# Optimization experiments

Hardware: AMD Instinct MI355X
Metric: run time of the kernel (lower is better)

The kernel has to match this reference:

```python
import jax, jax.numpy as jnp
import numpy as np
from jax import lax

V = 500000  # vocab
B = 4096    # batch_num (fixed at init via h0/c0)
E = 64      # embed_size_word
H = 64      # lstm hidden


def setup_inputs() -> dict:
    key = jax.random.key(0)
    ks = iter(jax.random.split(key, 40))
    nrm = lambda *s: 0.1 * jax.random.normal(next(ks), s, dtype=jnp.float32)
    x = jax.random.randint(next(ks), (912, B), 0, V).astype(jnp.float32)
    return dict(
        x=x,
        word_embed=nrm(V, E),
        lstm_Wih=nrm(4, 4 * H, E), lstm_Whh=nrm(4, 4 * H, H),
        lstm_bih=nrm(4, 4 * H), lstm_bhh=nrm(4, 4 * H),
        h0=nrm(4, B, H), c0=nrm(4, B, H),
        w_l=nrm(4, H, H), b_l=jnp.zeros((4, H, 1), jnp.float32),
        conv1_w=nrm(12, 1, 2, E), conv1_b=jnp.zeros((12,), jnp.float32),
        lin1_w=nrm(64, 24), lin1_b=jnp.zeros((64,), jnp.float32),
        conv2_w=nrm(12, 1, 2, E), conv2_b=jnp.zeros((12,), jnp.float32),
        lin2_w=nrm(64, 24), lin2_b=jnp.zeros((64,), jnp.float32),
        wide_w=nrm(64, 81), wide_b=jnp.zeros((64, 1), jnp.float32),
        cq_w=nrm(64, 64 * 7), cq_b=jnp.zeros((64, 1), jnp.float32),
        cqu_w=nrm(64, 128), cqu_b=jnp.zeros((64, 1), jnp.float32),
        dw_w=nrm(1, 64), dw_b=jnp.zeros((1, 1), jnp.float32),
    )


def _masked_mean(terms_f, table):
    # terms_f: [rows, B] float ids. Faithful to torch: L = sum(sign(all terms)),
    # L = L if L > 1 else 1, then mean over first min(L, rows) rows.
    rows = terms_f.shape[0]
    emb = table[terms_f.astype(jnp.int32)]                    # [rows, B, E]
    n = jnp.sum(jnp.sign(terms_f))
    L = jnp.minimum(jnp.where(n > 1, n, 1.0), float(rows))
    mask = (jnp.arange(rows, dtype=jnp.float32) < L)[:, None, None]
    return jnp.sum(emb * mask, axis=0) / L                    # [B, E]


def _lstm_last(x_seq, h0, c0, Wih, Whh, bih, bhh):
    # PyTorch LSTM (i,f,g,o gate order); returns last-step output h_T. x_seq: [T,B,E]
    def step(carry, xt):
        h, c = carry
        g = xt @ Wih.T + h @ Whh.T + bih + bhh                # [B, 4H]
        i, f, gg, o = jnp.split(g, 4, axis=-1)
        c = jax.nn.sigmoid(f) * c + jax.nn.sigmoid(i) * jnp.tanh(gg)
        h = jax.nn.sigmoid(o) * jnp.tanh(c)
        return (h, c), None
    (h, _), _ = lax.scan(step, (h0, c0), x_seq)
    return h                                                  # [B, H]


def reference(x, word_embed, lstm_Wih, lstm_Whh, lstm_bih, lstm_bhh, h0, c0, w_l, b_l,
              conv1_w, conv1_b, lin1_w, lin1_b, conv2_w, conv2_b, lin2_w, lin2_b,
              wide_w, wide_b, cq_w, cq_b, cqu_w, cqu_b, dw_w, dw_b):
    Bn = x.shape[1]
    wide_feat = x[:81]
    user_item_seq = x[81:276]
    query_feat = x[276:292]
    user_query_seq = x[292:462]
    query_item_query = x[462:562]
    user_query_item = x[562:662]
    user_item_query = x[662:812]
    query_user_item = x[812:]

    q_sum = _masked_mean(query_feat[:10], word_embed).T       # [64, B]

    def step_means(seg, chunk, term_rows):
        # split seg into 5 chunks of `chunk` rows, embed first `term_rows` rows per chunk
        chunks = seg.reshape(5, chunk, Bn)[:, :term_rows]     # [5, term_rows, B]
        return jax.vmap(lambda t: _masked_mean(t, word_embed))(chunks)  # [5, B, E]

    def lstm_stream(steps, i):
        h = _lstm_last(steps, h0[i], c0[i], lstm_Wih[i], lstm_Whh[i], lstm_bih[i], lstm_bhh[i])
        return jnp.tanh(w_l[i] @ h.T + b_l[i])                # [64, B]

    s1 = lstm_stream(step_means(user_item_seq[-65:], 13, 10), 0)
    s2 = lstm_stream(step_means(user_item_query[:50], 10, 5), 1)
    s3 = lstm_stream(step_means(user_query_item[-50:], 10, 5), 2)
    s4 = lstm_stream(step_means(user_query_seq[-65:], 13, 10), 3)

    def cnn_stream(steps, cw, cb, lw, lb):
        xi = steps.transpose(1, 0, 2)[:, None]                # [B, 1, 5, E]
        y = lax.conv_general_dilated(xi, cw, (1, 1), 'VALID',
                dimension_numbers=('NCHW', 'OIHW', 'NCHW')) + cb[None, :, None, None]
        y = jax.nn.relu(y)                                    # [B, 12, 4, 1]
        y = lax.reduce_window(y, -jnp.inf, lax.max, (1, 1, 2, 1), (1, 1, 2, 1), 'VALID')
        y = y.transpose(0, 2, 3, 1).reshape(Bn, 24)           # [B, 2*1*12]
        return jax.nn.relu(y @ lw.T + lb).T                   # [64, B]

    c1 = cnn_stream(step_means(query_item_query[-50:], 10, 5), conv1_w, conv1_b, lin1_w, lin1_b)
    c2 = cnn_stream(step_means(query_user_item[-50:], 10, 5), conv2_w, conv2_b, lin2_w, lin2_b)

    wide = jnp.tanh(wide_w @ wide_feat + wide_b)              # [64, B]
    q = jnp.tanh(cq_w @ jnp.concatenate([q_sum, s1, s2, s3, s4, c1, c2], 0) + cq_b)
    qw = jnp.tanh(cqu_w @ jnp.concatenate([q, wide], 0) + cqu_b)
    return dw_w @ qw + dw_b                                   # [1, B] logits
```

## Files before the change

### kernel.cpp

```cpp
#include <hip/hip_runtime.h>
#include <math.h>

#define BN 4096
typedef unsigned short u16;
typedef unsigned int   u32;
typedef short bfx8 __attribute__((ext_vector_type(8)));
typedef float fx4  __attribute__((ext_vector_type(4)));

__device__ const int c_base[31] = {
  276,
  211, 224, 237, 250, 263,
  662, 672, 682, 692, 702,
  612, 622, 632, 642, 652,
  397, 410, 423, 436, 449,
  512, 522, 532, 542, 552,
  862, 872, 882, 892, 902
};
__device__ const int c_rows[31] = {
  10,
  10,10,10,10,10,
  5,5,5,5,5,
  5,5,5,5,5,
  10,10,10,10,10,
  5,5,5,5,5,
  5,5,5,5,5
};

__device__ __forceinline__ u16 f2bf(float f){
  u32 u = __float_as_uint(f);
  return (u16)((u + 0x7FFFu + ((u >> 16) & 1u)) >> 16);
}
__device__ __forceinline__ float bf2f(u16 h){ return __uint_as_float(((u32)h) << 16); }
__device__ __forceinline__ float4 ld4(const float* p){ return *(const float4*)p; }
__device__ __forceinline__ float sigf(float v){ return 1.0f / (1.0f + __expf(-v)); }

extern "C" __global__ __launch_bounds__(256)
void setup_kernel(const float* __restrict__ x, int* __restrict__ cnt,
                  const float* __restrict__ Wih, const float* __restrict__ Whh,
                  const float* __restrict__ wl,  const float* __restrict__ bih,
                  const float* __restrict__ bhh,
                  const float* __restrict__ cqw, const float* __restrict__ cquw,
                  const float* __restrict__ ww,  const float* __restrict__ l1w,
                  const float* __restrict__ l2w,
                  u16* __restrict__ Wcb, u16* __restrict__ wlb,
                  float* __restrict__ bias_sum,
                  float* __restrict__ cqwT, float* __restrict__ cquwT,
                  float* __restrict__ wwT,  float* __restrict__ lwT){
  __shared__ int red[256];
  if (blockIdx.x < 248){
    const int c = blockIdx.x >> 3, part = blockIdx.x & 7;
    const int base = c_base[c], rows = c_rows[c];
    const int n_per = rows * 512;
    const int start = part * n_per;
    int s = 0;
    for (int i = start + threadIdx.x; i < start + n_per; i += 256){
      float v = x[(size_t)(base + (i >> 12)) * BN + (i & 4095)];
      s += (v > 0.f) ? 1 : ((v < 0.f) ? -1 : 0);
    }
    red[threadIdx.x] = s; __syncthreads();
    for (int off = 128; off > 0; off >>= 1){
      if (threadIdx.x < off) red[threadIdx.x] += red[threadIdx.x + off];
      __syncthreads();
    }
    if (threadIdx.x == 0) atomicAdd(&cnt[c], red[0]);
    return;
  }
  int idx = (blockIdx.x - 248) * 256 + threadIdx.x;
  if (idx < 131072){
    int s = idx >> 15, rem = idx & 32767, n = rem >> 7, k = rem & 127;
    float v = (k < 64) ? Wih[s*16384 + n*64 + k] : Whh[s*16384 + n*64 + (k-64)];
    Wcb[idx] = f2bf(v);
  } else if (idx < 147456){
    int j = idx - 131072;
    wlb[j] = f2bf(wl[j]);
  } else if (idx < 148480){
    int j = idx - 147456;
    bias_sum[j] = bih[j] + bhh[j];
  } else if (idx < 177152){
    int j = idx - 148480;
    int k = j >> 6, m = j & 63;
    cqwT[j] = cqw[m*448 + k];
  } else if (idx < 185344){
    int j = idx - 177152;
    int k = j >> 6, m = j & 63;
    cquwT[j] = cquw[m*128 + k];
  } else if (idx < 190528){
    int j = idx - 185344;
    int k = j >> 6, m = j & 63;
    wwT[j] = ww[m*81 + k];
  } else if (idx < 193600){
    int j = idx - 190528;
    int cs = j >= 1536;
    int r = j - (cs ? 1536 : 0);
    int k = r >> 6, m = r & 63;
    lwT[j] = (cs ? l2w : l1w)[m*24 + k];
  }
}

template<int ROWS>
__device__ __forceinline__ void means_body(const float* __restrict__ x,
                                           const float* __restrict__ we,
                                           float L, int base, int b0, int lane,
                                           float* m){
  float a0 = 0.f, a1 = 0.f, a2 = 0.f, a3 = 0.f;
  #pragma unroll
  for (int r = 0; r < ROWS; ++r){
    float4 iv = ld4(x + (size_t)(base + r) * BN + b0);
    float wr = ((float)r < L) ? 1.f : 0.f;
    a0 += wr * we[(size_t)(int)iv.x * 64 + lane];
    a1 += wr * we[(size_t)(int)iv.y * 64 + lane];
    a2 += wr * we[(size_t)(int)iv.z * 64 + lane];
    a3 += wr * we[(size_t)(int)iv.w * 64 + lane];
  }
  m[0] = a0 / L; m[1] = a1 / L; m[2] = a2 / L; m[3] = a3 / L;
}

extern "C" __global__ __launch_bounds__(256)
void means_kernel(const float* __restrict__ x, const float* __restrict__ we,
                  const int* __restrict__ cnt, u16* __restrict__ Mbf){
  const int c = blockIdx.x >> 8, tile = blockIdx.x & 255;
  const int w = threadIdx.x >> 6, lane = threadIdx.x & 63;
  const int b0 = tile * 16 + w * 4;
  const int base = c_base[c], rows = c_rows[c];
  const float L = fminf(fmaxf((float)cnt[c], 1.f), (float)rows);
  float m[4];
  if (rows == 5) means_body<5>(x, we, L, base, b0, lane, m);
  else          means_body<10>(x, we, L, base, b0, lane, m);
  #pragma unroll
  for (int j = 0; j < 4; ++j)
    Mbf[((size_t)c * BN + b0 + j) * 64 + lane] = f2bf(m[j]);
}

extern "C" __global__ __launch_bounds__(256, 1)
void lstm_kernel(const u16* __restrict__ Wcb, const u16* __restrict__ wlb,
                 const float* __restrict__ bias_sum, const u16* __restrict__ Mbf,
                 const float* __restrict__ h0, const float* __restrict__ c0,
                 const float* __restrict__ bl, float* __restrict__ S){
  __shared__ u16 Xh[64][136];

  const int tid = threadIdx.x, w = tid >> 6, lane = tid & 63;
  const int quad = lane >> 4, l0 = lane & 15;
  const int st = blockIdx.x & 3, tile = blockIdx.x >> 2, b0 = tile * 64;
  const int brow = 16 * w + l0;
  const u16* Wc = Wcb + (size_t)st * 32768;

  fx4 bias4[16];
  #pragma unroll
  for (int mt = 0; mt < 16; ++mt)
    bias4[mt] = *(const fx4*)(bias_sum + st*256 + mt*16 + quad*4);

  float cst[4][4];
  #pragma unroll
  for (int dc = 0; dc < 4; ++dc){
    float4 v = ld4(c0 + ((size_t)st*BN + b0 + brow)*64 + dc*16 + quad*4);
    cst[dc][0]=v.x; cst[dc][1]=v.y; cst[dc][2]=v.z; cst[dc][3]=v.w;
  }
  {
    const float* hp = h0 + ((size_t)st*BN + b0 + brow)*64 + quad*16;
    #pragma unroll
    for (int i = 0; i < 4; ++i){
      float4 v = ld4(hp + i*4);
      u32* dst = (u32*)&Xh[brow][64 + quad*16 + i*4];
      dst[0] = (u32)f2bf(v.x) | ((u32)f2bf(v.y) << 16);
      dst[1] = (u32)f2bf(v.z) | ((u32)f2bf(v.w) << 16);
    }
  }

  for (int t = 0; t < 5; ++t){
    {
      const u16* src = Mbf + ((size_t)(1 + st*5 + t)*BN + b0 + brow)*64 + quad*16;
      *(uint4*)&Xh[brow][quad*16]     = *(const uint4*)src;
      *(uint4*)&Xh[brow][quad*16 + 8] = *(const uint4*)(src + 8);
    }
    __syncthreads();

    fx4 acc[16];
    #pragma unroll
    for (int mt = 0; mt < 16; ++mt) acc[mt] = bias4[mt];
    #pragma unroll
    for (int kc = 0; kc < 4; ++kc){
      bfx8 bfr = *(const bfx8*)&Xh[brow][kc*32 + quad*8];
      #pragma unroll
      for (int mt = 0; mt < 16; ++mt){
        bfx8 afr = *(const bfx8*)(Wc + (size_t)(mt*16 + l0)*128 + kc*32 + quad*8);
        acc[mt] = __builtin_amdgcn_mfma_f32_16x16x32_bf16(afr, bfr, acc[mt], 0, 0, 0);
      }
    }
    #pragma unroll
    for (int dc = 0; dc < 4; ++dc){
      u16 hv[4];
      #pragma unroll
      for (int r = 0; r < 4; ++r){
        float ig = sigf(acc[dc][r]);
        float fg = sigf(acc[4 + dc][r]);
        float gg = tanhf(acc[8 + dc][r]);
        float og = sigf(acc[12 + dc][r]);
        float cc = fg * cst[dc][r] + ig * gg;
        cst[dc][r] = cc;
        hv[r] = f2bf(og * tanhf(cc));
      }
      u32* dst = (u32*)&Xh[brow][64 + dc*16 + quad*4];
      dst[0] = (u32)hv[0] | ((u32)hv[1] << 16);
      dst[1] = (u32)hv[2] | ((u32)hv[3] << 16);
    }
    __syncthreads();
  }

  fx4 acc2[4];
  #pragma unroll
  for (int mt = 0; mt < 4; ++mt){ acc2[mt].x=0.f; acc2[mt].y=0.f; acc2[mt].z=0.f; acc2[mt].w=0.f; }
  #pragma unroll
  for (int kc = 0; kc < 2; ++kc){
    bfx8 bfr = *(const bfx8*)&Xh[brow][64 + kc*32 + quad*8];
    #pragma unroll
    for (int mt = 0; mt < 4; ++mt){
      bfx8 afr = *(const bfx8*)(wlb + (size_t)st*4096 + (size_t)(mt*16 + l0)*64 + kc*32 + quad*8);
      acc2[mt] = __builtin_amdgcn_mfma_f32_16x16x32_bf16(afr, bfr, acc2[mt], 0, 0, 0);
    }
  }
  #pragma unroll
  for (int mt = 0; mt < 4; ++mt){
    fx4 blv = *(const fx4*)(bl + st*64 + mt*16 + quad*4);
    fx4 o;
    o.x = tanhf(acc2[mt].x + blv.x);
    o.y = tanhf(acc2[mt].y + blv.y);
    o.z = tanhf(acc2[mt].z + blv.z);
    o.w = tanhf(acc2[mt].w + blv.w);
    *(fx4*)(S + ((size_t)st*BN + b0 + brow)*64 + mt*16 + quad*4) = o;
  }
}

extern "C" __global__ __launch_bounds__(256)
void final_kernel(
    const float* __restrict__ x,   const u16* __restrict__ Mbf,
    const float* __restrict__ S,
    const float* __restrict__ c1w, const float* __restrict__ c1b,
    const float* __restrict__ c2w, const float* __restrict__ c2b,
    const float* __restrict__ l1b, const float* __restrict__ l2b,
    const float* __restrict__ wwT, const float* __restrict__ wb,
    const float* __restrict__ cqwT,const float* __restrict__ cqb,
    const float* __restrict__ cquwT,const float* __restrict__ cqub,
    const float* __restrict__ lwT, const float* __restrict__ dww,
    const float* __restrict__ dwb, float* __restrict__ out)
{
  __shared__ float cb[448][9];
  __shared__ float qwin[128][9];
  __shared__ float sm[5][64][9];
  __shared__ float co[48][9];
  __shared__ float cwS[12][130];
  __shared__ float red[32][8];

  const int tid = threadIdx.x;
  const int b   = tid & 7;
  const int mg  = tid >> 3;
  const int b0  = blockIdx.x * 8;

  {
    const int e = tid & 63, rr = tid >> 6;
    #pragma unroll
    for (int i = 0; i < 2; ++i){
      const int bb = rr*2 + i;
      cb[e][bb] = bf2f(Mbf[(size_t)(b0 + bb)*64 + e]);
      #pragma unroll
      for (int s = 0; s < 4; ++s)
        cb[64 + s*64 + e][bb] = S[((size_t)s*BN + b0 + bb)*64 + e];
    }
  }

  {
    float a0 = wb[mg*2], a1 = wb[mg*2+1];
    #pragma unroll 4
    for (int k = 0; k < 81; ++k){
      float xv = x[(size_t)k*BN + b0 + b];
      float2 wv = *(const float2*)(wwT + k*64 + mg*2);
      a0 += wv.x * xv; a1 += wv.y * xv;
    }
    qwin[64 + mg*2][b]     = tanhf(a0);
    qwin[64 + mg*2 + 1][b] = tanhf(a1);
  }

  for (int cs = 0; cs < 2; ++cs){
    const float* cw    = cs ? c2w : c1w;
    const float* cbias = cs ? c2b : c1b;
    const float* lb    = cs ? l2b : l1b;

    __syncthreads();
    {
      const int e = tid & 63, rr = tid >> 6;
      #pragma unroll
      for (int t = 0; t < 5; ++t)
        #pragma unroll
        for (int i = 0; i < 2; ++i){
          const int bb = rr*2 + i;
          sm[t][e][bb] = bf2f(Mbf[((size_t)(21 + cs*5 + t)*BN + b0 + bb)*64 + e]);
        }
      for (int r2 = tid; r2 < 1536; r2 += 256){
        const int o = r2 >> 7, j = r2 & 127;
        cwS[o][j] = cw[o*128 + j];
      }
    }
    __syncthreads();

    if (mg < 24){
      const int o = mg >> 1, hb = (mg & 1) * 2;
      float a0 = cbias[o], a1 = cbias[o];
      #pragma unroll 4
      for (int e = 0; e < 64; ++e){
        float w0 = cwS[o][e], w1 = cwS[o][64 + e];
        float s0 = sm[hb][e][b], s1 = sm[hb+1][e][b], s2 = sm[hb+2][e][b];
        a0 += w0*s0 + w1*s1;
        a1 += w0*s1 + w1*s2;
      }
      co[o*4 + hb][b]     = fmaxf(a0, 0.f);
      co[o*4 + hb + 1][b] = fmaxf(a1, 0.f);
    }
    __syncthreads();

    {
      float a0 = lb[mg*2], a1 = lb[mg*2+1];
      #pragma unroll
      for (int k = 0; k < 24; ++k){
        const int p = k >= 12, o = k - (p ? 12 : 0);
        float f = fmaxf(co[o*4 + 2*p][b], co[o*4 + 2*p + 1][b]);
        float2 lv = *(const float2*)(lwT + (cs*24 + k)*64 + mg*2);
        a0 += lv.x * f; a1 += lv.y * f;
      }
      cb[320 + cs*64 + mg*2][b]     = fmaxf(a0, 0.f);
      cb[320 + cs*64 + mg*2 + 1][b] = fmaxf(a1, 0.f);
    }
  }

  __syncthreads();
  {
    float a0 = cqb[mg*2], a1 = cqb[mg*2+1];
    #pragma unroll 8
    for (int k = 0; k < 448; ++k){
      float a = cb[k][b];
      float2 wv = *(const float2*)(cqwT + k*64 + mg*2);
      a0 += wv.x * a; a1 += wv.y * a;
    }
    qwin[mg*2][b]     = tanhf(a0);
    qwin[mg*2 + 1][b] = tanhf(a1);
  }
  __syncthreads();
  {
    float a0 = cqub[mg*2], a1 = cqub[mg*2+1];
    #pragma unroll 8
    for (int k = 0; k < 128; ++k){
      float a = qwin[k][b];
      float2 wv = *(const float2*)(cquwT + k*64 + mg*2);
      a0 += wv.x * a; a1 += wv.y * a;
    }
    float2 dv = *(const float2*)(dww + mg*2);
    red[mg][b] = dv.x * tanhf(a0) + dv.y * tanhf(a1);
  }
  __syncthreads();
  if (tid < 8){
    float s = dwb[0];
    #pragma unroll 8
    for (int g = 0; g < 32; ++g) s += red[g][tid];
    out[b0 + tid] = s;
  }
}

extern "C" void kernel_launch(void* const* d_in, const int* in_sizes, int n_in,
                              void* d_out, int out_size, void* d_ws, size_t ws_size,
                              hipStream_t stream) {
  const float* x    = (const float*)d_in[0];
  const float* we   = (const float*)d_in[1];
  const float* Wih  = (const float*)d_in[2];
  const float* Whh  = (const float*)d_in[3];
  const float* bihp = (const float*)d_in[4];
  const float* bhhp = (const float*)d_in[5];
  const float* h0   = (const float*)d_in[6];
  const float* c0   = (const float*)d_in[7];
  const float* wl   = (const float*)d_in[8];
  const float* bl   = (const float*)d_in[9];
  const float* c1w  = (const float*)d_in[10];
  const float* c1b  = (const float*)d_in[11];
  const float* l1w  = (const float*)d_in[12];
  const float* l1b  = (const float*)d_in[13];
  const float* c2w  = (const float*)d_in[14];
  const float* c2b  = (const float*)d_in[15];
  const float* l2w  = (const float*)d_in[16];
  const float* l2b  = (const float*)d_in[17];
  const float* ww   = (const float*)d_in[18];
  const float* wb   = (const float*)d_in[19];
  const float* cqw  = (const float*)d_in[20];
  const float* cqb  = (const float*)d_in[21];
  const float* cquw = (const float*)d_in[22];
  const float* cqub = (const float*)d_in[23];
  const float* dww  = (const float*)d_in[24];
  const float* dwb  = (const float*)d_in[25];

  char* ws = (char*)d_ws;
  int*   cnt   = (int*)ws;
  u16*   Mbf   = (u16*)(ws + 1024);
  u16*   Wcb   = (u16*)(ws + 16253952);
  u16*   wlb   = (u16*)(ws + 16516096);
  float* bias  = (float*)(ws + 16548864);
  float* S     = (float*)(ws + 16552960);
  float* cqwT  = (float*)(ws + 20747264);
  float* cquwT = (float*)(ws + 20861952);
  float* wwT   = (float*)(ws + 20894720);
  float* lwT   = (float*)(ws + 20915456);

  hipMemsetAsync(cnt, 0, 31 * sizeof(int), stream);
  setup_kernel<<<1005, 256, 0, stream>>>(x, cnt, Wih, Whh, wl, bihp, bhhp,
      cqw, cquw, ww, l1w, l2w, Wcb, wlb, bias, cqwT, cquwT, wwT, lwT);
  means_kernel<<<7936, 256, 0, stream>>>(x, we, cnt, Mbf);
  lstm_kernel<<<256, 256, 0, stream>>>(Wcb, wlb, bias, Mbf, h0, c0, bl, S);
  final_kernel<<<512, 256, 0, stream>>>(x, Mbf, S,
      c1w, c1b, c2w, c2b, l1b, l2b,
      wwT, wb, cqwT, cqb, cquwT, cqub, lwT, dww, dwb, (float*)d_out);
}
```

Baseline: 354.6 us.

## Restructure prep kernels, drop memset/atomics, widen means tiles, use fast tanh

```diff
diff --git a/kernel.cpp b/kernel.cpp
--- a/kernel.cpp
+++ b/kernel.cpp
@@ -32,40 +32,89 @@
 }
 __device__ __forceinline__ float bf2f(u16 h){ return __uint_as_float(((u32)h) << 16); }
 __device__ __forceinline__ float4 ld4(const float* p){ return *(const float4*)p; }
-__device__ __forceinline__ float sigf(float v){ return 1.0f / (1.0f + __expf(-v)); }
+__device__ __forceinline__ float frcp(float x){ return __builtin_amdgcn_rcpf(x); }
+__device__ __forceinline__ float sigf(float v){ return frcp(1.f + __expf(-v)); }
+__device__ __forceinline__ float tanhf_(float v){ return 1.f - 2.f*frcp(1.f + __expf(2.f*v)); }
 
 extern "C" __global__ __launch_bounds__(256)
-void setup_kernel(const float* __restrict__ x, int* __restrict__ cnt,
-                  const float* __restrict__ Wih, const float* __restrict__ Whh,
-                  const float* __restrict__ wl,  const float* __restrict__ bih,
-                  const float* __restrict__ bhh,
-                  const float* __restrict__ cqw, const float* __restrict__ cquw,
-                  const float* __restrict__ ww,  const float* __restrict__ l1w,
-                  const float* __restrict__ l2w,
-                  u16* __restrict__ Wcb, u16* __restrict__ wlb,
-                  float* __restrict__ bias_sum,
-                  float* __restrict__ cqwT, float* __restrict__ cquwT,
-                  float* __restrict__ wwT,  float* __restrict__ lwT){
+void count_kernel(const float* __restrict__ x, int* __restrict__ cnt8){
   __shared__ int red[256];
-  if (blockIdx.x < 248){
-    const int c = blockIdx.x >> 3, part = blockIdx.x & 7;
+  const int c = blockIdx.x >> 3, part = blockIdx.x & 7;
+  const int base = c_base[c], rows = c_rows[c];
+  const int n_per = rows * 512;
+  const int start = part * n_per;
+  int s = 0;
+  for (int i = start + threadIdx.x; i < start + n_per; i += 256){
+    float v = x[(size_t)(base + (i >> 12)) * BN + (i & 4095)];
+    s += (v > 0.f) ? 1 : ((v < 0.f) ? -1 : 0);
+  }
+  red[threadIdx.x] = s; __syncthreads();
+  for (int off = 128; off > 0; off >>= 1){
+    if (threadIdx.x < off) red[threadIdx.x] += red[threadIdx.x + off];
+    __syncthreads();
+  }
+  if (threadIdx.x == 0) cnt8[blockIdx.x] = red[0];
+}
+
+template<int ROWS>
+__device__ __forceinline__ void means_body8(const float* __restrict__ x,
+                                            const float* __restrict__ we,
+                                            float L, int base, int b0, int lane,
+                                            float* m){
+  float a[8];
+  #pragma unroll
+  for (int j = 0; j < 8; ++j) a[j] = 0.f;
+  #pragma unroll
+  for (int r = 0; r < ROWS; ++r){
+    float4 i0 = ld4(x + (size_t)(base + r) * BN + b0);
+    float4 i1 = ld4(x + (size_t)(base + r) * BN + b0 + 4);
+    float wr = ((float)r < L) ? 1.f : 0.f;
+    a[0] += wr * we[(size_t)(int)i0.x * 64 + lane];
+    a[1] += wr * we[(size_t)(int)i0.y * 64 + lane];
+    a[2] += wr * we[(size_t)(int)i0.z * 64 + lane];
+    a[3] += wr * we[(size_t)(int)i0.w * 64 + lane];
+    a[4] += wr * we[(size_t)(int)i1.x * 64 + lane];
+    a[5] += wr * we[(size_t)(int)i1.y * 64 + lane];
+    a[6] += wr * we[(size_t)(int)i1.z * 64 + lane];
+    a[7] += wr * we[(size_t)(int)i1.w * 64 + lane];
+  }
+  float rL = 1.f / L;
+  #pragma unroll
+  for (int j = 0; j < 8; ++j) m[j] = a[j] * rL;
+}
+
+extern "C" __global__ __launch_bounds__(256)
+void meansprep_kernel(const float* __restrict__ x, const float* __restrict__ we,
+                      const int* __restrict__ cnt8, u16* __restrict__ Mbf,
+                      const float* __restrict__ Wih, const float* __restrict__ Whh,
+                      const float* __restrict__ wl,  const float* __restrict__ bih,
+                      const float* __restrict__ bhh,
+                      const float* __restrict__ cqw, const float* __restrict__ cquw,
+                      const float* __restrict__ ww,  const float* __restrict__ l1w,
+                      const float* __restrict__ l2w,
+                      u16* __restrict__ Wcb, u16* __restrict__ wlb,
+                      float* __restrict__ bias_sum,
+                      float* __restrict__ cqwT, float* __restrict__ cquwT,
+                      float* __restrict__ wwT,  float* __restrict__ lwT){
+  const int blk = blockIdx.x;
+  if (blk < 3968){
+    const int c = blk >> 7, tile = blk & 127;
+    const int w = threadIdx.x >> 6, lane = threadIdx.x & 63;
+    const int b0 = tile * 32 + w * 8;
     const int base = c_base[c], rows = c_rows[c];
-    const int n_per = rows * 512;
-    const int start = part * n_per;
-    int s = 0;
-    for (int i = start + threadIdx.x; i < start + n_per; i += 256){
-      float v = x[(size_t)(base + (i >> 12)) * BN + (i & 4095)];
-      s += (v > 0.f) ? 1 : ((v < 0.f) ? -1 : 0);
-    }
-    red[threadIdx.x] = s; __syncthreads();
-    for (int off = 128; off > 0; off >>= 1){
-      if (threadIdx.x < off) red[threadIdx.x] += red[threadIdx.x + off];
-      __syncthreads();
-    }
-    if (threadIdx.x == 0) atomicAdd(&cnt[c], red[0]);
+    int n = 0;
+    #pragma unroll
+    for (int p = 0; p < 8; ++p) n += cnt8[c*8 + p];
+    const float L = fminf(fmaxf((float)n, 1.f), (float)rows);
+    float m[8];
+    if (rows == 5) means_body8<5>(x, we, L, base, b0, lane, m);
+    else          means_body8<10>(x, we, L, base, b0, lane, m);
+    #pragma unroll
+    for (int j = 0; j < 8; ++j)
+      Mbf[((size_t)c * BN + b0 + j) * 64 + lane] = f2bf(m[j]);
     return;
   }
-  int idx = (blockIdx.x - 248) * 256 + threadIdx.x;
+  int idx = (blk - 3968) * 256 + threadIdx.x;
   if (idx < 131072){
     int s = idx >> 15, rem = idx & 32767, n = rem >> 7, k = rem & 127;
     float v = (k < 64) ? Wih[s*16384 + n*64 + k] : Whh[s*16384 + n*64 + (k-64)];
@@ -97,40 +146,6 @@
   }
 }
 
-template<int ROWS>
-__device__ __forceinline__ void means_body(const float* __restrict__ x,
-                                           const float* __restrict__ we,
-                                           float L, int base, int b0, int lane,
-                                           float* m){
-  float a0 = 0.f, a1 = 0.f, a2 = 0.f, a3 = 0.f;
-  #pragma unroll
-  for (int r = 0; r < ROWS; ++r){
-    float4 iv = ld4(x + (size_t)(base + r) * BN + b0);
-    float wr = ((float)r < L) ? 1.f : 0.f;
-    a0 += wr * we[(size_t)(int)iv.x * 64 + lane];
-    a1 += wr * we[(size_t)(int)iv.y * 64 + lane];
-    a2 += wr * we[(size_t)(int)iv.z * 64 + lane];
-    a3 += wr * we[(size_t)(int)iv.w * 64 + lane];
-  }
-  m[0] = a0 / L; m[1] = a1 / L; m[2] = a2 / L; m[3] = a3 / L;
-}
-
-extern "C" __global__ __launch_bounds__(256)
-void means_kernel(const float* __restrict__ x, const float* __restrict__ we,
-                  const int* __restrict__ cnt, u16* __restrict__ Mbf){
-  const int c = blockIdx.x >> 8, tile = blockIdx.x & 255;
-  const int w = threadIdx.x >> 6, lane = threadIdx.x & 63;
-  const int b0 = tile * 16 + w * 4;
-  const int base = c_base[c], rows = c_rows[c];
-  const float L = fminf(fmaxf((float)cnt[c], 1.f), (float)rows);
-  float m[4];
-  if (rows == 5) means_body<5>(x, we, L, base, b0, lane, m);
-  else          means_body<10>(x, we, L, base, b0, lane, m);
-  #pragma unroll
-  for (int j = 0; j < 4; ++j)
-    Mbf[((size_t)c * BN + b0 + j) * 64 + lane] = f2bf(m[j]);
-}
-
 extern "C" __global__ __launch_bounds__(256, 1)
 void lstm_kernel(const u16* __restrict__ Wcb, const u16* __restrict__ wlb,
                  const float* __restrict__ bias_sum, const u16* __restrict__ Mbf,
@@ -193,11 +208,11 @@
       for (int r = 0; r < 4; ++r){
         float ig = sigf(acc[dc][r]);
         float fg = sigf(acc[4 + dc][r]);
-        float gg = tanhf(acc[8 + dc][r]);
+        float gg = tanhf_(acc[8 + dc][r]);
         float og = sigf(acc[12 + dc][r]);
         float cc = fg * cst[dc][r] + ig * gg;
         cst[dc][r] = cc;
-        hv[r] = f2bf(og * tanhf(cc));
+        hv[r] = f2bf(og * tanhf_(cc));
       }
       u32* dst = (u32*)&Xh[brow][64 + dc*16 + quad*4];
       dst[0] = (u32)hv[0] | ((u32)hv[1] << 16);
@@ -222,10 +237,10 @@
   for (int mt = 0; mt < 4; ++mt){
     fx4 blv = *(const fx4*)(bl + st*64 + mt*16 + quad*4);
     fx4 o;
-    o.x = tanhf(acc2[mt].x + blv.x);
-    o.y = tanhf(acc2[mt].y + blv.y);
-    o.z = tanhf(acc2[mt].z + blv.z);
-    o.w = tanhf(acc2[mt].w + blv.w);
+    o.x = tanhf_(acc2[mt].x + blv.x);
+    o.y = tanhf_(acc2[mt].y + blv.y);
+    o.z = tanhf_(acc2[mt].z + blv.z);
+    o.w = tanhf_(acc2[mt].w + blv.w);
     *(fx4*)(S + ((size_t)st*BN + b0 + brow)*64 + mt*16 + quad*4) = o;
   }
 }
@@ -275,8 +290,8 @@
       float2 wv = *(const float2*)(wwT + k*64 + mg*2);
       a0 += wv.x * xv; a1 += wv.y * xv;
     }
-    qwin[64 + mg*2][b]     = tanhf(a0);
-    qwin[64 + mg*2 + 1][b] = tanhf(a1);
+    qwin[64 + mg*2][b]     = tanhf_(a0);
+    qwin[64 + mg*2 + 1][b] = tanhf_(a1);
   }
 
   for (int cs = 0; cs < 2; ++cs){
@@ -339,8 +354,8 @@
       float2 wv = *(const float2*)(cqwT + k*64 + mg*2);
       a0 += wv.x * a; a1 += wv.y * a;
     }
-    qwin[mg*2][b]     = tanhf(a0);
-    qwin[mg*2 + 1][b] = tanhf(a1);
+    qwin[mg*2][b]     = tanhf_(a0);
+    qwin[mg*2 + 1][b] = tanhf_(a1);
   }
   __syncthreads();
   {
@@ -352,7 +367,7 @@
       a0 += wv.x * a; a1 += wv.y * a;
     }
     float2 dv = *(const float2*)(dww + mg*2);
-    red[mg][b] = dv.x * tanhf(a0) + dv.y * tanhf(a1);
+    red[mg][b] = dv.x * tanhf_(a0) + dv.y * tanhf_(a1);
   }
   __syncthreads();
   if (tid < 8){
@@ -394,7 +409,7 @@
   const float* dwb  = (const float*)d_in[25];
 
   char* ws = (char*)d_ws;
-  int*   cnt   = (int*)ws;
+  int*   cnt8  = (int*)ws;
   u16*   Mbf   = (u16*)(ws + 1024);
   u16*   Wcb   = (u16*)(ws + 16253952);
   u16*   wlb   = (u16*)(ws + 16516096);
@@ -405,10 +420,10 @@
   float* wwT   = (float*)(ws + 20894720);
   float* lwT   = (float*)(ws + 20915456);
 
-  hipMemsetAsync(cnt, 0, 31 * sizeof(int), stream);
-  setup_kernel<<<1005, 256, 0, stream>>>(x, cnt, Wih, Whh, wl, bihp, bhhp,
-      cqw, cquw, ww, l1w, l2w, Wcb, wlb, bias, cqwT, cquwT, wwT, lwT);
-  means_kernel<<<7936, 256, 0, stream>>>(x, we, cnt, Mbf);
+  count_kernel<<<248, 256, 0, stream>>>(x, cnt8);
+  meansprep_kernel<<<4725, 256, 0, stream>>>(x, we, cnt8, Mbf,
+      Wih, Whh, wl, bihp, bhhp, cqw, cquw, ww, l1w, l2w,
+      Wcb, wlb, bias, cqwT, cquwT, wwT, lwT);
   lstm_kernel<<<256, 256, 0, stream>>>(Wcb, wlb, bias, Mbf, h0, c0, bl, S);
   final_kernel<<<512, 256, 0, stream>>>(x, Mbf, S,
       c1w, c1b, c2w, c2b, l1b, l2b,
```

Measured after the change: 342.0 us. 1.04x faster.
